# Performance work log

Hardware: AMD Instinct MI355X
Metric: run time of the kernel (lower is better)

Reference implementation:

```python
import jax, jax.numpy as jnp
import numpy as np

BOOST_STRENGTH = 1.0  # from init kwargs, already >= 0


def setup_inputs() -> dict:
    key = jax.random.key(0)
    k1, k2 = jax.random.split(key)
    B, C, H, W = 64, 128, 56, 56
    x = jax.random.normal(k1, (B, C, H, W), dtype=jnp.float32)
    # duty cycles are running activation frequencies in [0, 1]
    duty_cycles = jax.random.uniform(k2, (1, C, 1, 1), dtype=jnp.float32)
    k = 40141  # round(0.1 * C*H*W)
    return {"x": x, "duty_cycles": duty_cycles, "k": k}


def reference(x, duty_cycles, k):
    B = x.shape[0]
    n = x.shape[1] * x.shape[2] * x.shape[3]
    target_density = jnp.float32(k / n)
    # boosting only selects winners; original (unboosted) values are kept
    boost_factors = jnp.exp((target_density - duty_cycles) * BOOST_STRENGTH)
    boosted = (x * boost_factors).reshape(B, -1)   # [B, n]
    flat_x = x.reshape(B, -1)                      # [B, n]
    _, idx = jax.lax.top_k(boosted, k)             # [B, k]
    winners = jnp.take_along_axis(flat_x, idx, axis=1)  # original values at winning units
    res = jnp.zeros_like(flat_x).at[jnp.arange(B)[:, None], idx].set(winners)
    return res.reshape(x.shape)
```

## Files before the change

kernel.cpp:

```cpp
#include <hip/hip_runtime.h>
#include <stdint.h>

#define BB 64
#define CC 128
#define HW 3136
#define NPR (CC * HW)
#define NF4 (NPR / 4)
#define F4CH (HW / 4)
#define SS 2048
#define SSTRIDE 49
#define MARGIN 128

typedef float vf4 __attribute__((ext_vector_type(4)));

#define THI_OFF 0
#define TLO_OFF 256
#define CHI_OFF 512
#define CNT_OFF 768
#define CAND_OFF 4096

__device__ __forceinline__ uint32_t tokey(float b) {
    uint32_t u = __float_as_uint(b);
    return u ^ (uint32_t)(((int32_t)u >> 31) | 0x80000000);
}
__device__ __forceinline__ float fromkey(uint32_t k) {
    uint32_t u = (k & 0x80000000u) ? (k ^ 0x80000000u) : ~k;
    return __uint_as_float(u);
}

__device__ __forceinline__ float boostf(const float* dc, int c, int K) {
    float td = (float)((double)K / (double)NPR);
    float d = td - dc[c];
    return (float)exp((double)d);
}

__device__ uint32_t select32(const uint32_t* kreg, uint32_t m,
                             uint32_t* whist , uint32_t* sufs, int* sh_d) {
    int tid = threadIdx.x;
    int wid = tid >> 6;
    uint32_t prefix = 0, mask = 0, remaining = m;
    for (int shift = 24; shift >= 0; shift -= 8) {
        for (int i = tid; i < 16 * 256; i += 1024) whist[i] = 0;
        __syncthreads();
        #pragma unroll
        for (int i = 0; i < 8; i++) {
            uint32_t v = kreg[i];
            if ((v & mask) == prefix)
                atomicAdd(&whist[(wid << 8) + ((v >> shift) & 255u)], 1u);
        }
        __syncthreads();
        if (tid < 256) {
            uint32_t s = 0;
            for (int w = 0; w < 16; w++) s += whist[(w << 8) + tid];
            sufs[tid] = s;
        }
        __syncthreads();
        for (int off = 1; off < 256; off <<= 1) {
            uint32_t add = 0;
            if (tid < 256 && tid + off < 256) add = sufs[tid + off];
            __syncthreads();
            if (tid < 256) sufs[tid] += add;
            __syncthreads();
        }
        if (tid < 256) {
            uint32_t sd = sufs[tid], sn = (tid < 255) ? sufs[tid + 1] : 0u;
            if (sd >= remaining && sn < remaining) *sh_d = tid;
        }
        __syncthreads();
        int d = *sh_d;
        uint32_t cumG = (d < 255) ? sufs[d + 1] : 0u;
        prefix |= ((uint32_t)d << shift);
        mask |= (0xFFu << shift);
        remaining -= cumG;
        __syncthreads();
    }
    return prefix;
}

__device__ unsigned long long select64(const unsigned long long* cp, uint32_t cnt,
                                       uint32_t E, uint32_t* hh, uint32_t* sufs,
                                       unsigned long long* lbuf, uint32_t* scnt,
                                       int* sh_d, int* sh_done) {
    int tid = threadIdx.x, nt = blockDim.x;
    unsigned long long prefix = 0ull, mask = 0ull, thr = 0ull;
    uint32_t remaining = E, csize = cnt;
    bool compacted = false;
    if (tid == 0) *sh_done = 0;
    __syncthreads();
    for (int shift = 56; shift >= 0; shift -= 8) {
        if (tid < 256) hh[tid] = 0;
        __syncthreads();
        if (!compacted) {
            for (uint32_t s = tid; s < cnt; s += nt) {
                unsigned long long v = cp[s];
                if ((v & mask) == prefix)
                    atomicAdd(&hh[(uint32_t)(v >> shift) & 255u], 1u);
            }
        } else {
            for (uint32_t s = tid; s < csize; s += nt)
                atomicAdd(&hh[(uint32_t)(lbuf[s] >> shift) & 255u], 1u);
        }
        __syncthreads();
        if (tid < 256) sufs[tid] = hh[tid];
        __syncthreads();
        for (int off = 1; off < 256; off <<= 1) {
            uint32_t add = 0;
            if (tid < 256 && tid + off < 256) add = sufs[tid + off];
            __syncthreads();
            if (tid < 256) sufs[tid] += add;
            __syncthreads();
        }
        if (tid < 256) {
            uint32_t sd = sufs[tid], sn = (tid < 255) ? sufs[tid + 1] : 0u;
            if (sd >= remaining && sn < remaining) *sh_d = tid;
        }
        __syncthreads();
        int d = *sh_d;
        uint32_t cumG = (d < 255) ? sufs[d + 1] : 0u;
        uint32_t binC = sufs[d] - cumG;
        unsigned long long npref = prefix | ((unsigned long long)(uint32_t)d << shift);
        bool done_ = (sufs[d] == remaining);
        if (done_) { thr = npref; if (tid == 0) *sh_done = 1; }
        remaining -= cumG;
        __syncthreads();
        if (!*sh_done && binC <= 4096u && shift > 0) {
            if (tid == 0) *scnt = 0;
            unsigned long long keep[8]; int nk = 0;
            if (compacted) {
                for (uint32_t s = tid; s < csize; s += nt) {
                    unsigned long long v = lbuf[s];
                    if (((uint32_t)(v >> shift) & 255u) == (uint32_t)d && nk < 8)
                        keep[nk++] = v;
                }
            }
            __syncthreads();
            if (!compacted) {
                for (uint32_t s = tid; s < cnt; s += nt) {
                    unsigned long long v = cp[s];
                    if ((v & mask) == prefix &&
                        ((uint32_t)(v >> shift) & 255u) == (uint32_t)d)
                        lbuf[atomicAdd(scnt, 1u)] = v;
                }
            } else if (nk > 0) {
                uint32_t p = atomicAdd(scnt, (uint32_t)nk);
                for (int i = 0; i < nk; i++) lbuf[p + i] = keep[i];
            }
            __syncthreads();
            csize = binC;
            compacted = true;
        }
        prefix = npref;
        mask |= (0xFFull << shift);
        if (*sh_done) break;
    }
    __syncthreads();
    if (!*sh_done) thr = prefix;
    return thr;
}

__global__ __launch_bounds__(1024) void k_sample(const float* __restrict__ x,
                                                 const float* __restrict__ dc,
                                                 const int* __restrict__ kptr,
                                                 uint32_t* __restrict__ thi,
                                                 uint32_t* __restrict__ tlo) {
    __shared__ float sbf[CC];
    __shared__ uint32_t whist[16 * 256];
    __shared__ uint32_t sufs[256];
    __shared__ int sh_d;
    int row = blockIdx.x, tid = threadIdx.x;
    int K = *kptr;
    if (tid < CC) sbf[tid] = boostf(dc, tid, K);
    __syncthreads();
    const float4* xp = (const float4*)(x + (size_t)row * NPR);
    uint32_t kreg[8];
    #pragma unroll
    for (int h = 0; h < 2; h++) {
        int u = tid + h * 1024;
        float4 v = xp[(size_t)u * SSTRIDE];
        float f = sbf[u >> 4];
        kreg[4*h+0] = tokey(v.x * f); kreg[4*h+1] = tokey(v.y * f);
        kreg[4*h+2] = tokey(v.z * f); kreg[4*h+3] = tokey(v.w * f);
    }
    int S = SS * 4;
    int m_mid = (int)(((long long)K * S) / NPR);
    int m_hi = m_mid - MARGIN; if (m_hi < 1) m_hi = 1;
    int m_lo = m_mid + MARGIN; if (m_lo > S) m_lo = S;
    uint32_t t1 = select32(kreg, (uint32_t)m_hi, whist, sufs, &sh_d);
    __syncthreads();
    uint32_t t2 = select32(kreg, (uint32_t)m_lo, whist, sufs, &sh_d);
    if (tid == 0) { thi[row] = t1; tlo[row] = t2; }
}

__device__ __forceinline__ void push_cand(bool isc, unsigned long long packed,
                                          uint32_t* lcnt, unsigned long long* lbuf,
                                          uint32_t* counters, unsigned long long* cand,
                                          int row, int cap) {
    unsigned long long ball = __ballot(isc);
    uint32_t tot = (uint32_t)__popcll(ball);
    if (tot == 0) return;
    uint32_t lo = (uint32_t)ball, hi = (uint32_t)(ball >> 32);
    uint32_t lanepre = __builtin_amdgcn_mbcnt_hi(hi, __builtin_amdgcn_mbcnt_lo(lo, 0));
    int leader = __ffsll((unsigned long long)ball) - 1;
    uint32_t base = 0;
    if (isc && lanepre == 0) base = atomicAdd(lcnt, tot);
    base = __shfl(base, leader, 64);
    if (isc) {
        uint32_t pos = base + lanepre;
        if (pos < 4096u) lbuf[pos] = packed;
        else {
            uint32_t gp = atomicAdd(&counters[row], 1u);
            if ((int)gp < cap) cand[(size_t)row * cap + gp] = packed;
        }
    }
}

__global__ __launch_bounds__(256) void k_stream(const float* __restrict__ x,
                                                const float* __restrict__ dc,
                                                const int* __restrict__ kptr,
                                                const uint32_t* __restrict__ thi,
                                                const uint32_t* __restrict__ tlo,
                                                float* __restrict__ out,
                                                unsigned long long* __restrict__ cand,
                                                uint32_t* __restrict__ counters,
                                                uint32_t* __restrict__ chi,
                                                int cap) {
    int row = blockIdx.x >> 4;
    int c0 = (blockIdx.x & 15) * 8;
    float Bhi = fromkey(thi[row]);
    float Blo = fromkey(tlo[row]);

    __shared__ float sbf[8];
    __shared__ uint32_t lcnt, gbase;
    __shared__ unsigned long long lbuf[4096];
    __shared__ uint32_t red[256];
    if (threadIdx.x == 0) lcnt = 0;
    if (threadIdx.x < 8) sbf[threadIdx.x] = boostf(dc, c0 + threadIdx.x, *kptr);
    __syncthreads();

    size_t base = (size_t)row * NPR + (size_t)c0 * HW;
    const float4* xp = (const float4*)(x + base);
    vf4* op = (vf4*)(out + base);
    int jbase = c0 * HW;
    const int nf4 = 8 * HW / 4;
    uint32_t myhi = 0;

    int t = threadIdx.x;
    for (; t + 256 < nf4; t += 512) {
        float4 a = xp[t];
        float4 b = xp[t + 256];
        float fa = sbf[t / F4CH];
        float fb = sbf[(t + 256) / F4CH];
        vf4 oa, ob;
        float* ai = (float*)&a;
        float* bi = (float*)&b;
        #pragma unroll
        for (int q = 0; q < 4; q++) {
            float xv = ai[q];
            float bv = xv * fa;
            bool win = bv > Bhi;
            myhi += win;
            oa[q] = win ? xv : 0.0f;
            bool isc = (bv > Blo) && !win;
            uint32_t j = (uint32_t)(jbase + 4 * t + q);
            unsigned long long packed = ((unsigned long long)tokey(bv) << 32) | (uint32_t)(~j);
            push_cand(isc, packed, &lcnt, lbuf, counters, cand, row, cap);
        }
        #pragma unroll
        for (int q = 0; q < 4; q++) {
            float xv = bi[q];
            float bv = xv * fb;
            bool win = bv > Bhi;
            myhi += win;
            ob[q] = win ? xv : 0.0f;
            bool isc = (bv > Blo) && !win;
            uint32_t j = (uint32_t)(jbase + 4 * (t + 256) + q);
            unsigned long long packed = ((unsigned long long)tokey(bv) << 32) | (uint32_t)(~j);
            push_cand(isc, packed, &lcnt, lbuf, counters, cand, row, cap);
        }
        __builtin_nontemporal_store(oa, &op[t]);
        __builtin_nontemporal_store(ob, &op[t + 256]);
    }
    if (t < nf4) {
        float4 a = xp[t];
        float fa = sbf[t / F4CH];
        vf4 oa;
        float* ai = (float*)&a;
        #pragma unroll
        for (int q = 0; q < 4; q++) {
            float xv = ai[q];
            float bv = xv * fa;
            bool win = bv > Bhi;
            myhi += win;
            oa[q] = win ? xv : 0.0f;
            bool isc = (bv > Blo) && !win;
            uint32_t j = (uint32_t)(jbase + 4 * t + q);
            unsigned long long packed = ((unsigned long long)tokey(bv) << 32) | (uint32_t)(~j);
            push_cand(isc, packed, &lcnt, lbuf, counters, cand, row, cap);
        }
        __builtin_nontemporal_store(oa, &op[t]);
    }
    __syncthreads();
    uint32_t m = lcnt < 4096u ? lcnt : 4096u;
    if (threadIdx.x == 0) gbase = atomicAdd(&counters[row], m);
    __syncthreads();
    for (uint32_t i = threadIdx.x; i < m; i += 256) {
        uint32_t pos = gbase + i;
        if ((int)pos < cap) cand[(size_t)row * cap + pos] = lbuf[i];
    }
    red[threadIdx.x] = myhi;
    __syncthreads();
    for (int off = 128; off > 0; off >>= 1) {
        if ((int)threadIdx.x < off) red[threadIdx.x] += red[threadIdx.x + off];
        __syncthreads();
    }
    if (threadIdx.x == 0) atomicAdd(&chi[row], red[0]);
}

__global__ __launch_bounds__(1024) void k_final(const float* __restrict__ x,
                                                const float* __restrict__ dc,
                                                const int* __restrict__ kptr,
                                                const uint32_t* __restrict__ thi,
                                                const uint32_t* __restrict__ tlo,
                                                float* __restrict__ out,
                                                unsigned long long* __restrict__ cand,
                                                const uint32_t* __restrict__ counters,
                                                const uint32_t* __restrict__ chi,
                                                int cap) {
    __shared__ uint32_t bh[4096];
    __shared__ uint32_t cs[1024];
    __shared__ unsigned long long lbuf[4096];
    __shared__ float sbf[CC];
    __shared__ uint32_t scnt;
    __shared__ int sh_d, sh_done, sh_b;
    __shared__ uint32_t sh_r;
    __shared__ unsigned long long sh_thr;
    int row = blockIdx.x, tid = threadIdx.x;
    int K = *kptr;
    uint32_t cnt = counters[row], c_hi = chi[row];
    uint32_t Thi = thi[row], Tlo = tlo[row];
    long long Ell = (long long)K - (long long)c_hi;
    unsigned long long* cp = cand + (size_t)row * cap;
    const float* xr = x + (size_t)row * NPR;
    float* orow = out + (size_t)row * NPR;

    bool ok = (Ell >= 0) && (Ell <= (long long)cnt) && ((int)cnt <= cap) && (Thi > Tlo);
    if (ok) {
        if (Ell == 0) return;
        uint32_t E = (uint32_t)Ell;
        uint32_t R = Thi - Tlo;
        unsigned long long scale = (4096ULL << 32) / R;
        for (int i = tid; i < 4096; i += 1024) bh[i] = 0;
        __syncthreads();
        for (uint32_t s = tid; s < cnt; s += 1024) {
            uint32_t key = (uint32_t)(cp[s] >> 32);
            uint32_t rel = key - Tlo - 1;
            uint32_t bin = (uint32_t)(((unsigned long long)rel * scale) >> 32);
            if (bin > 4095u) bin = 4095u;
            atomicAdd(&bh[bin], 1u);
        }
        __syncthreads();
        int hi = 4095 - 4 * tid;
        uint32_t s4 = bh[hi] + bh[hi-1] + bh[hi-2] + bh[hi-3];
        cs[tid] = s4;
        __syncthreads();
        for (int off = 1; off < 1024; off <<= 1) {
            uint32_t v = (tid >= off) ? cs[tid - off] : 0u;
            __syncthreads();
            cs[tid] += v;
            __syncthreads();
        }
        uint32_t incl = cs[tid], excl = incl - s4;
        if (excl < E && incl >= E) {
            uint32_t cum = excl;
            for (int j = 0; j < 4; j++) {
                int b = hi - j;
                uint32_t h = bh[b];
                if (cum + h >= E) { sh_b = b; sh_r = E - cum; break; }
                cum += h;
            }
        }
        __syncthreads();
        int bstar = sh_b;
        uint32_t r = sh_r;
        uint32_t mm = bh[bstar];
        unsigned long long thr;
        if (mm <= 4096u) {
            if (tid == 0) scnt = 0;
            __syncthreads();
            for (uint32_t s = tid; s < cnt; s += 1024) {
                unsigned long long v = cp[s];
                uint32_t key = (uint32_t)(v >> 32);
                uint32_t rel = key - Tlo - 1;
                uint32_t bin = (uint32_t)(((unsigned long long)rel * scale) >> 32);
                if (bin > 4095u) bin = 4095u;
                if ((int)bin == bstar) lbuf[atomicAdd(&scnt, 1u)] = v;
            }
            __syncthreads();
            for (uint32_t i = tid; i < mm; i += 1024) {
                unsigned long long vi = lbuf[i];
                uint32_t above = 0;
                for (uint32_t j2 = 0; j2 < mm; j2++) above += (lbuf[j2] > vi);
                if (above == r - 1) sh_thr = vi;
            }
            __syncthreads();
            thr = sh_thr;
        } else {
            thr = select64(cp, cnt, E, bh, cs, lbuf, &scnt, &sh_d, &sh_done);
        }
        for (uint32_t s = tid; s < cnt; s += 1024) {
            unsigned long long v = cp[s];
            if (v >= thr) { uint32_t j = ~(uint32_t)v; orow[j] = xr[j]; }
        }
        return;
    }

    uint32_t* lh = (uint32_t*)lbuf;
    if (tid < CC) sbf[tid] = boostf(dc, tid, K);
    for (int i = tid; i < 8192; i += 1024) lh[i] = 0;
    __syncthreads();
    const float4* xp = (const float4*)xr;
    for (int t = tid; t < NF4; t += 1024) {
        float4 v = xp[t];
        float f = sbf[t / F4CH];
        atomicAdd(&lh[tokey(v.x * f) >> 19], 1u);
        atomicAdd(&lh[tokey(v.y * f) >> 19], 1u);
        atomicAdd(&lh[tokey(v.z * f) >> 19], 1u);
        atomicAdd(&lh[tokey(v.w * f) >> 19], 1u);
    }
    __syncthreads();
    {
        int hi = 8191 - 8 * tid;
        uint32_t s = 0;
        for (int j = 0; j < 8; j++) s += lh[hi - j];
        cs[tid] = s;
        __syncthreads();
        for (int off = 1; off < 1024; off <<= 1) {
            uint32_t v = (tid >= off) ? cs[tid - off] : 0u;
            __syncthreads();
            cs[tid] += v;
            __syncthreads();
        }
        uint32_t incl = cs[tid], excl = incl - s;
        if (excl < (uint32_t)K && incl >= (uint32_t)K) {
            uint32_t cum = excl;
            for (int j = 0; j < 8; j++) {
                int b = hi - j;
                uint32_t h = lh[b];
                if (cum + h >= (uint32_t)K) { sh_b = b; sh_r = (uint32_t)K - cum; break; }
                cum += h;
            }
        }
    }
    __syncthreads();
    int bstar = sh_b;
    uint32_t E2 = sh_r;
    if (tid == 0) scnt = 0;
    __syncthreads();
    for (int t = tid; t < NF4; t += 1024) {
        float4 v = xp[t];
        float f = sbf[t / F4CH];
        vf4 o;
        float* vi = (float*)&v;
        #pragma unroll
        for (int q = 0; q < 4; q++) {
            float xv = vi[q];
            uint32_t key = tokey(xv * f);
            int bin = (int)(key >> 19);
            o[q] = (bin > bstar) ? xv : 0.0f;
            if (bin == bstar) {
                uint32_t j = (uint32_t)(4 * t + q);
                unsigned long long packed = ((unsigned long long)key << 32) | (uint32_t)(~j);
                uint32_t p = atomicAdd(&scnt, 1u);
                if ((int)p < cap) cp[p] = packed;
            }
        }
        ((vf4*)orow)[t] = o;
    }
    __syncthreads();
    uint32_t cnt2 = scnt;
    if ((int)cnt2 > cap) cnt2 = (uint32_t)cap;
    unsigned long long thr = select64(cp, cnt2, E2, bh, cs, lbuf, &scnt, &sh_d, &sh_done);
    for (uint32_t s = tid; s < cnt2; s += 1024) {
        unsigned long long v = cp[s];
        if (v >= thr) { uint32_t j = ~(uint32_t)v; orow[j] = xr[j]; }
    }
}

extern "C" void kernel_launch(void* const* d_in, const int* in_sizes, int n_in,
                              void* d_out, int out_size, void* d_ws, size_t ws_size,
                              hipStream_t stream) {
    const float* x  = (const float*)d_in[0];
    const float* dc = (const float*)d_in[1];
    const int* kptr = (const int*)d_in[2];
    float* out = (float*)d_out;

    char* ws = (char*)d_ws;
    uint32_t* thi      = (uint32_t*)(ws + THI_OFF);
    uint32_t* tlo      = (uint32_t*)(ws + TLO_OFF);
    uint32_t* chi      = (uint32_t*)(ws + CHI_OFF);
    uint32_t* counters = (uint32_t*)(ws + CNT_OFF);
    unsigned long long* cand = (unsigned long long*)(ws + CAND_OFF);

    size_t cap_sz = (ws_size > CAND_OFF) ? (ws_size - CAND_OFF) / ((size_t)BB * 8) : 0;
    if (cap_sz > 65536) cap_sz = 65536;
    int cap = (int)cap_sz;

    (void)hipMemsetAsync(ws, 0, 4096, stream);
    k_sample<<<BB, 1024, 0, stream>>>(x, dc, kptr, thi, tlo);
    k_stream<<<BB * 16, 256, 0, stream>>>(x, dc, kptr, thi, tlo, out, cand, counters, chi, cap);
    k_final<<<BB, 1024, 0, stream>>>(x, dc, kptr, thi, tlo, out, cand, counters, chi, cap);
}
```

Measured before the change: 277.1 us.

## Split threshold selection across blocks, sample contiguously, prefetch stream loads

The sampling kernel now runs two blocks per row, each computing one of the two thresholds (hi/lo) instead of one block computing both in sequence. It reads a contiguous 16-float4 chunk per channel instead of a strided gather, and the radix select stops one 8-bit pass early, which makes the thresholds coarser. The stream kernel is restructured with explicit software prefetch of the next pair of float4 loads, and the memset is shrunk to cover only the counters. The contiguous sample is less spatially representative and the truncated select can widen the candidate band, so more work may land in the final kernel.

```diff
diff --git a/kernel.cpp b/kernel.cpp
--- a/kernel.cpp
+++ b/kernel.cpp
@@ -7,8 +7,6 @@
 #define NPR (CC * HW)
 #define NF4 (NPR / 4)
 #define F4CH (HW / 4)
-#define SS 2048
-#define SSTRIDE 49
 #define MARGIN 128
 
 typedef float vf4 __attribute__((ext_vector_type(4)));
@@ -39,7 +37,7 @@
     int tid = threadIdx.x;
     int wid = tid >> 6;
     uint32_t prefix = 0, mask = 0, remaining = m;
-    for (int shift = 24; shift >= 0; shift -= 8) {
+    for (int shift = 24; shift >= 8; shift -= 8) {
         for (int i = tid; i < 16 * 256; i += 1024) whist[i] = 0;
         __syncthreads();
         #pragma unroll
@@ -167,7 +165,8 @@
     __shared__ uint32_t whist[16 * 256];
     __shared__ uint32_t sufs[256];
     __shared__ int sh_d;
-    int row = blockIdx.x, tid = threadIdx.x;
+    int row = blockIdx.x >> 1, which = blockIdx.x & 1;
+    int tid = threadIdx.x;
     int K = *kptr;
     if (tid < CC) sbf[tid] = boostf(dc, tid, K);
     __syncthreads();
@@ -175,20 +174,20 @@
     uint32_t kreg[8];
     #pragma unroll
     for (int h = 0; h < 2; h++) {
-        int u = tid + h * 1024;
-        float4 v = xp[(size_t)u * SSTRIDE];
-        float f = sbf[u >> 4];
+        int s = tid + h * 1024;
+        int c = s >> 4, i = s & 15;
+        float4 v = xp[c * F4CH + i];
+        float f = sbf[c];
         kreg[4*h+0] = tokey(v.x * f); kreg[4*h+1] = tokey(v.y * f);
         kreg[4*h+2] = tokey(v.z * f); kreg[4*h+3] = tokey(v.w * f);
     }
-    int S = SS * 4;
+    int S = 8192;
     int m_mid = (int)(((long long)K * S) / NPR);
-    int m_hi = m_mid - MARGIN; if (m_hi < 1) m_hi = 1;
-    int m_lo = m_mid + MARGIN; if (m_lo > S) m_lo = S;
-    uint32_t t1 = select32(kreg, (uint32_t)m_hi, whist, sufs, &sh_d);
-    __syncthreads();
-    uint32_t t2 = select32(kreg, (uint32_t)m_lo, whist, sufs, &sh_d);
-    if (tid == 0) { thi[row] = t1; tlo[row] = t2; }
+    int m = which ? (m_mid + MARGIN) : (m_mid - MARGIN);
+    if (m < 1) m = 1;
+    if (m > S) m = S;
+    uint32_t t1 = select32(kreg, (uint32_t)m, whist, sufs, &sh_d);
+    if (tid == 0) { if (which) tlo[row] = t1; else thi[row] = t1; }
 }
 
 __device__ __forceinline__ void push_cand(bool isc, unsigned long long packed,
@@ -241,64 +240,42 @@
     const float4* xp = (const float4*)(x + base);
     vf4* op = (vf4*)(out + base);
     int jbase = c0 * HW;
-    const int nf4 = 8 * HW / 4;
+    int tid = threadIdx.x;
     uint32_t myhi = 0;
 
-    int t = threadIdx.x;
-    for (; t + 256 < nf4; t += 512) {
-        float4 a = xp[t];
-        float4 b = xp[t + 256];
-        float fa = sbf[t / F4CH];
-        float fb = sbf[(t + 256) / F4CH];
-        vf4 oa, ob;
-        float* ai = (float*)&a;
-        float* bi = (float*)&b;
+    auto proc = [&](int t, float4 v) {
+        float f = sbf[t / F4CH];
+        vf4 o;
+        float* vi = (float*)&v;
         #pragma unroll
         for (int q = 0; q < 4; q++) {
-            float xv = ai[q];
-            float bv = xv * fa;
+            float xv = vi[q];
+            float bv = xv * f;
             bool win = bv > Bhi;
             myhi += win;
-            oa[q] = win ? xv : 0.0f;
+            o[q] = win ? xv : 0.0f;
             bool isc = (bv > Blo) && !win;
             uint32_t j = (uint32_t)(jbase + 4 * t + q);
-            unsigned long long packed = ((unsigned long long)tokey(bv) << 32) | (uint32_t)(~j);
+            unsigned long long packed =
+                ((unsigned long long)tokey(bv) << 32) | (uint32_t)(~j);
             push_cand(isc, packed, &lcnt, lbuf, counters, cand, row, cap);
         }
-        #pragma unroll
-        for (int q = 0; q < 4; q++) {
-            float xv = bi[q];
-            float bv = xv * fb;
-            bool win = bv > Bhi;
-            myhi += win;
-            ob[q] = win ? xv : 0.0f;
-            bool isc = (bv > Blo) && !win;
-            uint32_t j = (uint32_t)(jbase + 4 * (t + 256) + q);
-            unsigned long long packed = ((unsigned long long)tokey(bv) << 32) | (uint32_t)(~j);
-            push_cand(isc, packed, &lcnt, lbuf, counters, cand, row, cap);
-        }
-        __builtin_nontemporal_store(oa, &op[t]);
-        __builtin_nontemporal_store(ob, &op[t + 256]);
-    }
-    if (t < nf4) {
-        float4 a = xp[t];
-        float fa = sbf[t / F4CH];
-        vf4 oa;
-        float* ai = (float*)&a;
-        #pragma unroll
-        for (int q = 0; q < 4; q++) {
-            float xv = ai[q];
-            float bv = xv * fa;
-            bool win = bv > Bhi;
-            myhi += win;
-            oa[q] = win ? xv : 0.0f;
-            bool isc = (bv > Blo) && !win;
-            uint32_t j = (uint32_t)(jbase + 4 * t + q);
-            unsigned long long packed = ((unsigned long long)tokey(bv) << 32) | (uint32_t)(~j);
-            push_cand(isc, packed, &lcnt, lbuf, counters, cand, row, cap);
-        }
-        __builtin_nontemporal_store(oa, &op[t]);
-    }
+        __builtin_nontemporal_store(o, &op[t]);
+    };
+
+    float4 a = xp[tid];
+    float4 b = xp[tid + 256];
+    for (int p = 0; p < 12; ++p) {
+        int t0 = p * 512 + tid;
+        float4 a2, b2;
+        if (p < 11) { a2 = xp[t0 + 512]; b2 = xp[t0 + 768]; }
+        else if (tid < 128) { a2 = xp[6144 + tid]; }
+        proc(t0, a);
+        proc(t0 + 256, b);
+        a = a2; b = b2;
+    }
+    if (tid < 128) proc(6144 + tid, a);
+
     __syncthreads();
     uint32_t m = lcnt < 4096u ? lcnt : 4096u;
     if (threadIdx.x == 0) gbase = atomicAdd(&counters[row], m);
@@ -505,8 +482,8 @@
     if (cap_sz > 65536) cap_sz = 65536;
     int cap = (int)cap_sz;
 
-    (void)hipMemsetAsync(ws, 0, 4096, stream);
-    k_sample<<<BB, 1024, 0, stream>>>(x, dc, kptr, thi, tlo);
+    (void)hipMemsetAsync(ws + CHI_OFF, 0, 512, stream);
+    k_sample<<<BB * 2, 1024, 0, stream>>>(x, dc, kptr, thi, tlo);
     k_stream<<<BB * 16, 256, 0, stream>>>(x, dc, kptr, thi, tlo, out, cand, counters, chi, cap);
     k_final<<<BB, 1024, 0, stream>>>(x, dc, kptr, thi, tlo, out, cand, counters, chi, cap);
 }
```

Measured after the change: 267.7 us. -3.4%, faster.
